# Kernel tuning notes

Hardware: AMD Instinct MI355X
Metric: run time of the kernel (lower is better)

Reference implementation:

```python
import jax, jax.numpy as jnp
import numpy as np
import math

B, S, E, H = 2, 2048, 1024, 16
D = E // H          # d_k = 64 = n_qubits_per_head
F = 1024            # ffn_dim; MUST equal E for the original mixing to broadcast
LN_EPS = 1e-5


def _layernorm(x, g, b):
    m = jnp.mean(x, axis=-1, keepdims=True)
    v = jnp.var(x, axis=-1, keepdims=True)
    return (x - m) / jnp.sqrt(v + LN_EPS) * g + b


def _circuit_expvals(x):
    # Closed form of the variational circuit: RY(x_i) on wire i, RZ(theta_i),
    # CNOT chain (i -> i+1), measure PauliZ on each wire.
    # RZ is diagonal (no effect on Z probs); CNOT chain makes bit_i the XOR of
    # bits 0..i, so <Z_i> = prod_{j<=i} cos(x_j).
    return jnp.cumprod(jnp.cos(x), axis=-1)


def setup_inputs() -> dict:
    key = jax.random.key(0)
    ks = jax.random.split(key, 18)
    sc = 0.02
    inp = {
        "x": jax.random.normal(ks[0], (B, S, E), jnp.float32),
        "mask": jnp.ones((B, S), jnp.int32),
        "wq": jax.random.normal(ks[1], (E, E), jnp.float32) * sc,
        "wk": jax.random.normal(ks[2], (E, E), jnp.float32) * sc,
        "wv": jax.random.normal(ks[3], (E, E), jnp.float32) * sc,
        "wo": jax.random.normal(ks[4], (E, E), jnp.float32) * sc,
        "attn_param": jax.random.normal(ks[5], (D,), jnp.float32),   # RZ angles (no effect on expvals)
        "attn_qw": jnp.float32(0.5),
        "w1": jax.random.normal(ks[6], (E, F), jnp.float32) * sc,
        "b1": jnp.zeros((F,), jnp.float32),
        "w2": jax.random.normal(ks[7], (F, E), jnp.float32) * sc,
        "b2": jnp.zeros((E,), jnp.float32),
        "ffn_param": jax.random.normal(ks[8], (E,), jnp.float32),    # RZ angles (no effect on expvals)
        "ffn_qw": jnp.float32(0.5),
        "ln1_g": jnp.ones((E,), jnp.float32),
        "ln1_b": jnp.zeros((E,), jnp.float32),
        "ln2_g": jnp.ones((E,), jnp.float32),
        "ln2_b": jnp.zeros((E,), jnp.float32),
    }
    return inp


def reference(x, mask, wq, wk, wv, wo, attn_param, attn_qw,
              w1, b1, w2, b2, ffn_param, ffn_qw,
              ln1_g, ln1_b, ln2_g, ln2_b):
    b, s, _ = x.shape
    # ---- quantum attention sublayer (dropout inactive / eval mode) ----
    q = (x @ wq).reshape(b, s, H, D).transpose(0, 2, 1, 3)  # [b,h,s,d]
    k = (x @ wk).reshape(b, s, H, D).transpose(0, 2, 1, 3)
    v = (x @ wv).reshape(b, s, H, D).transpose(0, 2, 1, 3)
    scores = jnp.einsum("bhqd,bhkd->bhqk", q, k) / math.sqrt(D)
    scores = jnp.where(mask[:, None, None, :] == 0, -jnp.inf, scores)
    attn = jax.nn.softmax(scores, axis=-1)
    classical = jnp.einsum("bhqk,bhkd->bhqd", attn, v)
    quantum = _circuit_expvals(q)                             # [b,h,s,d]
    wgt = jax.nn.sigmoid(attn_qw)
    out = wgt * quantum + (1.0 - wgt) * classical
    attn_out = out.transpose(0, 2, 1, 3).reshape(b, s, E) @ wo
    x1 = _layernorm(x + attn_out, ln1_g, ln1_b)
    # ---- quantum feed-forward sublayer ----
    classical2 = jax.nn.relu(x1 @ w1 + b1)                    # [b,s,F]
    quantum2 = _circuit_expvals(x1)                           # [b,s,E] (E==F)
    wgt2 = jax.nn.sigmoid(ffn_qw)
    h = wgt2 * quantum2 + (1.0 - wgt2) * classical2
    ffn_out = h @ w2 + b2
    return _layernorm(x1 + ffn_out, ln2_g, ln2_b)
```

## Files before the change

kernel.cpp:

```cpp
#include <hip/hip_runtime.h>
#include <hip/hip_bf16.h>
#include <cmath>
#include <cstdint>


typedef __bf16 bf16_t;
typedef __bf16 bf16x8 __attribute__((ext_vector_type(8)));
typedef float f32x4 __attribute__((ext_vector_type(4)));
typedef unsigned short u16x4 __attribute__((ext_vector_type(4)));

#define DEV_INLINE __device__ __forceinline__
#define MB 1048576

DEV_INLINE void gload16(const void* g, void* lds) {
  __builtin_amdgcn_global_load_lds(
      (const __attribute__((address_space(1))) unsigned int*)g,
      (__attribute__((address_space(3))) unsigned int*)lds, 16, 0, 0);
}

DEV_INLINE unsigned short bf16_bits(float f) {
  bf16_t b = (bf16_t)f;
  return __builtin_bit_cast(unsigned short, b);
}

__global__ __launch_bounds__(256) void prep_kernel(
    const float* __restrict__ x, const float* __restrict__ wq,
    const float* __restrict__ wk, const float* __restrict__ wv,
    const float* __restrict__ wo, const float* __restrict__ w1,
    const float* __restrict__ w2, bf16_t* __restrict__ xc,
    bf16_t* __restrict__ wqkvT, bf16_t* __restrict__ wT3) {
  __shared__ bf16_t t[32][33];
  const int bid = blockIdx.x;
  if (bid < 2048) {
    const size_t i0 = ((size_t)bid * 256 + threadIdx.x) * 8;
    bf16x8 v;
#pragma unroll
    for (int j = 0; j < 8; ++j) v[j] = (bf16_t)x[i0 + j];
    *(bf16x8*)(xc + i0) = v;
    return;
  }
  const int grp = (bid - 2048) / 3072;
  const int tcb = (bid - 2048) - grp * 3072;
  const int mi = tcb >> 10;
  const float* src;
  bf16_t* dst;
  if (grp == 0) {
    src = (mi == 0) ? wq : (mi == 1) ? wk : wv;
    dst = wqkvT;
  } else {
    src = (mi == 0) ? wo : (mi == 1) ? w1 : w2;
    dst = wT3;
  }
  const int rem = tcb & 1023;
  const int bx = (rem & 31) * 32, by = (rem >> 5) * 32;
  const int tx = threadIdx.x & 31, ty = threadIdx.x >> 5;
#pragma unroll
  for (int i = 0; i < 4; ++i)
    t[ty + i * 8][tx] = (bf16_t)src[(size_t)(by + ty + i * 8) * 1024 + bx + tx];
  __syncthreads();
#pragma unroll
  for (int i = 0; i < 4; ++i)
    dst[(size_t)(mi * 1024 + bx + ty + i * 8) * 1024 + by + tx] = t[tx][ty + i * 8];
}

__global__ __launch_bounds__(256) void qkvvt_kernel(
    const bf16_t* __restrict__ xc, const bf16_t* __restrict__ wqkvT,
    bf16_t* __restrict__ qb, bf16_t* __restrict__ kb,
    bf16_t* __restrict__ vTb) {
  constexpr int K = 1024, BK = 64;
  __shared__ __align__(16) bf16_t As[128 * BK];
  __shared__ __align__(16) bf16_t Bs[128 * BK];

  const int tid = threadIdx.x;
  const int w = tid >> 6, lane = tid & 63;
  const int quad = lane >> 4, tc = lane & 15;
  const int bid = blockIdx.x;
  const int isqk = (bid < 512);
  int m0, n0;
  const bf16_t *Ab, *Bb;
  if (isqk) {
    n0 = (bid & 15) * 128;
    m0 = (bid >> 4) * 128;
    Ab = xc + (size_t)m0 * K;
    Bb = wqkvT + (size_t)n0 * K;
  } else {
    const int t = bid - 512;
    n0 = (t & 31) * 128;
    m0 = (t >> 5) * 128;
    Ab = wqkvT + (size_t)(2 * 1024 * 1024) + (size_t)m0 * K;
    Bb = xc + (size_t)n0 * K;
  }
  const int wm = (w >> 1) * 64, wn = (w & 1) * 64;
  const int srow = lane >> 3, scol = (lane & 7) * 8;

  f32x4 acc[4][4] = {};

  for (int k0 = 0; k0 < K; k0 += BK) {
    __syncthreads();
#pragma unroll
    for (int it = 0; it < 4; ++it) {
      const int rbase = w * 32 + it * 8;
      gload16(Ab + (size_t)(rbase + srow) * K + k0 + scol, &As[rbase * BK]);
      gload16(Bb + (size_t)(rbase + srow) * K + k0 + scol, &Bs[rbase * BK]);
    }
    __syncthreads();
#pragma unroll
    for (int ks = 0; ks < 2; ++ks) {
      bf16x8 af[4], bfv[4];
#pragma unroll
      for (int i = 0; i < 4; ++i)
        af[i] = *(const bf16x8*)&As[(wm + i * 16 + tc) * BK + ks * 32 + quad * 8];
#pragma unroll
      for (int j = 0; j < 4; ++j)
        bfv[j] = *(const bf16x8*)&Bs[(wn + j * 16 + tc) * BK + ks * 32 + quad * 8];
#pragma unroll
      for (int i = 0; i < 4; ++i)
#pragma unroll
        for (int j = 0; j < 4; ++j)
          acc[i][j] = __builtin_amdgcn_mfma_f32_16x16x32_bf16(af[i], bfv[j],
                                                              acc[i][j], 0, 0, 0);
    }
  }

#pragma unroll
  for (int i = 0; i < 4; ++i) {
#pragma unroll
    for (int j = 0; j < 4; ++j) {
      const int row0 = m0 + wm + i * 16 + quad * 4;
      const int col = n0 + wn + j * 16 + tc;
      if (isqk) {
        const int part = col >> 10, e = col & 1023, hh = e >> 6, d = e & 63;
        bf16_t* dst = part ? kb : qb;
#pragma unroll
        for (int r = 0; r < 4; ++r) {
          const int row = row0 + r;
          const int b = row >> 11, s = row & 2047;
          dst[((size_t)(b * 16 + hh) * 2048 + s) * 64 + d] = (bf16_t)acc[i][j][r];
        }
      } else {
        const int b = col >> 11, s = col & 2047;
#pragma unroll
        for (int r = 0; r < 4; ++r) {
          vTb[((size_t)(b * 1024 + row0 + r)) * 2048 + s] = (bf16_t)acc[i][j][r];
        }
      }
    }
  }
}

enum { EPI_WO = 2, EPI_W1 = 3, EPI_W2 = 4 };

template <int EPI>
__global__ __launch_bounds__(256) void gemm_bt_kernel(
    const bf16_t* __restrict__ A, const bf16_t* __restrict__ Bt,
    void* __restrict__ o0, const float* __restrict__ auxf,
    const bf16_t* __restrict__ auxb, const float* __restrict__ bias,
    const float* __restrict__ scal) {
  constexpr int K = 1024, BK = 64;
  __shared__ __align__(16) bf16_t As[64 * BK];
  __shared__ __align__(16) bf16_t Bs[64 * BK];

  const int tid = threadIdx.x;
  const int w = tid >> 6, lane = tid & 63;
  const int quad = lane >> 4, tc = lane & 15;
  const int m0 = blockIdx.y * 64, n0 = blockIdx.x * 64;
  const int wm = (w >> 1) * 32, wn = (w & 1) * 32;
  const int srow = lane >> 3, scol = (lane & 7) * 8;

  f32x4 acc[2][2] = {};

  const bf16_t* Ab = A + (size_t)m0 * K;
  const bf16_t* Bb = Bt + (size_t)n0 * K;

  for (int k0 = 0; k0 < K; k0 += BK) {
    __syncthreads();
#pragma unroll
    for (int it = 0; it < 2; ++it) {
      const int rbase = w * 16 + it * 8;
      gload16(Ab + (size_t)(rbase + srow) * K + k0 + scol, &As[rbase * BK]);
      gload16(Bb + (size_t)(rbase + srow) * K + k0 + scol, &Bs[rbase * BK]);
    }
    __syncthreads();
#pragma unroll
    for (int ks = 0; ks < 2; ++ks) {
      bf16x8 af[2], bfv[2];
#pragma unroll
      for (int i = 0; i < 2; ++i)
        af[i] = *(const bf16x8*)&As[(wm + i * 16 + tc) * BK + ks * 32 + quad * 8];
#pragma unroll
      for (int j = 0; j < 2; ++j)
        bfv[j] = *(const bf16x8*)&Bs[(wn + j * 16 + tc) * BK + ks * 32 + quad * 8];
#pragma unroll
      for (int i = 0; i < 2; ++i)
#pragma unroll
        for (int j = 0; j < 2; ++j)
          acc[i][j] = __builtin_amdgcn_mfma_f32_16x16x32_bf16(af[i], bfv[j],
                                                              acc[i][j], 0, 0, 0);
    }
  }

  float wsig = 0.f;
  if (EPI == EPI_W1) wsig = 1.f / (1.f + __expf(-scal[0]));

#pragma unroll
  for (int i = 0; i < 2; ++i) {
#pragma unroll
    for (int j = 0; j < 2; ++j) {
      const int row0 = m0 + wm + i * 16 + quad * 4;
      const int col = n0 + wn + j * 16 + tc;
      if (EPI == EPI_WO) {
#pragma unroll
        for (int r = 0; r < 4; ++r) {
          const int row = row0 + r;
          ((float*)o0)[(size_t)row * 1024 + col] =
              acc[i][j][r] + auxf[(size_t)row * 1024 + col];
        }
      } else if (EPI == EPI_W1) {
#pragma unroll
        for (int r = 0; r < 4; ++r) {
          const int row = row0 + r;
          float c = fmaxf(acc[i][j][r] + bias[col], 0.f);
          const float qv = (float)auxb[(size_t)row * 1024 + col];
          ((bf16_t*)o0)[(size_t)row * 1024 + col] =
              (bf16_t)(wsig * qv + (1.f - wsig) * c);
        }
      } else {
#pragma unroll
        for (int r = 0; r < 4; ++r) {
          const int row = row0 + r;
          ((float*)o0)[(size_t)row * 1024 + col] =
              acc[i][j][r] + bias[col] + (float)auxb[(size_t)row * 1024 + col];
        }
      }
    }
  }
}

__global__ __launch_bounds__(256) void attn_kernel(
    const bf16_t* __restrict__ q, const bf16_t* __restrict__ k,
    const bf16_t* __restrict__ vT, const float* __restrict__ aqw,
    bf16_t* __restrict__ out) {
  constexpr int S = 2048, LDK = 72;
  __shared__ __align__(16) bf16_t Ks[64 * LDK];
  __shared__ __align__(16) bf16_t Vs[64 * LDK];
  __shared__ __align__(16) bf16_t Ps[4][32 * LDK];
  __shared__ bf16_t Ql[128 * LDK];
  __shared__ float segp[128][4];

  const int tid = threadIdx.x, w = tid >> 6, lane = tid & 63;
  const int quad = lane >> 4, tc = lane & 15;
  const int bh = blockIdx.y, q0 = blockIdx.x * 128;
  const bf16_t* qg = q + ((size_t)bh * S + q0) * 64;
  const bf16_t* kg = k + (size_t)bh * S * 64;
  const bf16_t* vg = vT + (size_t)bh * 64 * S;

  const int strow = tid >> 2, stcol = (tid & 3) * 16;

  bf16x8 pk0 = *(const bf16x8*)(kg + (size_t)strow * 64 + stcol);
  bf16x8 pk1 = *(const bf16x8*)(kg + (size_t)strow * 64 + stcol + 8);
  bf16x8 pv0 = *(const bf16x8*)(vg + (size_t)strow * S + stcol);
  bf16x8 pv1 = *(const bf16x8*)(vg + (size_t)strow * S + stcol + 8);

  {
    float c[2][16];
    const int ss = tid & 3;
#pragma unroll
    for (int pass = 0; pass < 2; ++pass) {
      const int rr = pass * 64 + (tid >> 2);
      const bf16_t* qr = qg + rr * 64 + ss * 16;
      float p = 1.f;
#pragma unroll
      for (int j2 = 0; j2 < 16; ++j2) {
        c[pass][j2] = __cosf((float)qr[j2]);
        p *= c[pass][j2];
      }
      segp[rr][ss] = p;
    }
    __syncthreads();
#pragma unroll
    for (int pass = 0; pass < 2; ++pass) {
      const int rr = pass * 64 + (tid >> 2);
      float pre = 1.f;
      for (int u = 0; u < ss; ++u) pre *= segp[rr][u];
#pragma unroll
      for (int j2 = 0; j2 < 16; ++j2) {
        pre *= c[pass][j2];
        Ql[rr * LDK + ss * 16 + j2] = (bf16_t)pre;
      }
    }
  }

  bf16x8 aq[2][2];
#pragma unroll
  for (int qs = 0; qs < 2; ++qs) {
    const int qrow = w * 32 + qs * 16 + tc;
#pragma unroll
    for (int ks = 0; ks < 2; ++ks) {
      bf16x8 t = *(const bf16x8*)(qg + qrow * 64 + ks * 32 + quad * 8);
#pragma unroll
      for (int e = 0; e < 8; ++e) t[e] = (bf16_t)((float)t[e] * 0.18033688f);
      aq[qs][ks] = t;
    }
  }

  float lacc[2] = {0.f, 0.f};
  f32x4 o[2][4] = {};
  bf16_t* Pw = Ps[w];

  for (int kt = 0; kt < S; kt += 64) {
    __syncthreads();
    *(bf16x8*)&Ks[strow * LDK + stcol] = pk0;
    *(bf16x8*)&Ks[strow * LDK + stcol + 8] = pk1;
    *(bf16x8*)&Vs[strow * LDK + stcol] = pv0;
    *(bf16x8*)&Vs[strow * LDK + stcol + 8] = pv1;
    if (kt + 64 < S) {
      const int nk = kt + 64;
      pk0 = *(const bf16x8*)(kg + (size_t)(nk + strow) * 64 + stcol);
      pk1 = *(const bf16x8*)(kg + (size_t)(nk + strow) * 64 + stcol + 8);
      pv0 = *(const bf16x8*)(vg + (size_t)strow * S + nk + stcol);
      pv1 = *(const bf16x8*)(vg + (size_t)strow * S + nk + stcol + 8);
    }
    __syncthreads();

    f32x4 sf[2][4] = {};
#pragma unroll
    for (int ks = 0; ks < 2; ++ks) {
#pragma unroll
      for (int nt = 0; nt < 4; ++nt) {
        bf16x8 ak = *(const bf16x8*)&Ks[(nt * 16 + tc) * LDK + ks * 32 + quad * 8];
        sf[0][nt] = __builtin_amdgcn_mfma_f32_16x16x32_bf16(ak, aq[0][ks], sf[0][nt], 0, 0, 0);
        sf[1][nt] = __builtin_amdgcn_mfma_f32_16x16x32_bf16(ak, aq[1][ks], sf[1][nt], 0, 0, 0);
      }
    }

#pragma unroll
    for (int qs = 0; qs < 2; ++qs) {
#pragma unroll
      for (int nt = 0; nt < 4; ++nt) {
        u16x4 pk;
        float ps = 0.f;
#pragma unroll
        for (int r = 0; r < 4; ++r) {
          const float p = __builtin_amdgcn_exp2f(sf[qs][nt][r]);
          ps += p;
          pk[r] = bf16_bits(p);
        }
        lacc[qs] += ps;
        *(u16x4*)&Pw[(qs * 16 + tc) * LDK + nt * 16 + quad * 4] = pk;
      }
    }
    asm volatile("s_waitcnt lgkmcnt(0)" ::: "memory");

#pragma unroll
    for (int ks = 0; ks < 2; ++ks) {
      bf16x8 ap0 = *(const bf16x8*)&Pw[tc * LDK + ks * 32 + quad * 8];
      bf16x8 ap1 = *(const bf16x8*)&Pw[(16 + tc) * LDK + ks * 32 + quad * 8];
#pragma unroll
      for (int j = 0; j < 4; ++j) {
        bf16x8 bv = *(const bf16x8*)&Vs[(j * 16 + tc) * LDK + ks * 32 + quad * 8];
        o[0][j] = __builtin_amdgcn_mfma_f32_16x16x32_bf16(ap0, bv, o[0][j], 0, 0, 0);
        o[1][j] = __builtin_amdgcn_mfma_f32_16x16x32_bf16(ap1, bv, o[1][j], 0, 0, 0);
      }
    }
  }

#pragma unroll
  for (int qs = 0; qs < 2; ++qs) {
    lacc[qs] += __shfl_xor(lacc[qs], 16, 64);
    lacc[qs] += __shfl_xor(lacc[qs], 32, 64);
  }

  const float wsig = 1.f / (1.f + __expf(-aqw[0]));
  const int b = bh >> 4, h = bh & 15;
#pragma unroll
  for (int qs = 0; qs < 2; ++qs) {
#pragma unroll
    for (int r = 0; r < 4; ++r) {
      const int lr = quad * 4 + r;
      const float linv = 1.f / __shfl(lacc[qs], lr, 64);
      const int lrow = w * 32 + qs * 16 + lr;
      const int sg = q0 + lrow;
#pragma unroll
      for (int j = 0; j < 4; ++j) {
        const int d = j * 16 + tc;
        const float cl = o[qs][j][r] * linv;
        const float qv = (float)Ql[lrow * LDK + d];
        out[((size_t)(b * 2048 + sg)) * 1024 + h * 64 + d] =
            (bf16_t)(wsig * qv + (1.f - wsig) * cl);
      }
    }
  }
}

__global__ __launch_bounds__(256) void ln1scan_kernel(
    const float* __restrict__ res, const float* __restrict__ g,
    const float* __restrict__ bta, bf16_t* __restrict__ x1,
    bf16_t* __restrict__ q2) {
  const int row = blockIdx.x;
  const int tid = threadIdx.x, w = tid >> 6, lane = tid & 63;
  f32x4 v = *(const f32x4*)&res[(size_t)row * 1024 + tid * 4];
  float s = v[0] + v[1] + v[2] + v[3];
  float sq = v[0] * v[0] + v[1] * v[1] + v[2] * v[2] + v[3] * v[3];
#pragma unroll
  for (int off = 32; off >= 1; off >>= 1) {
    s += __shfl_xor(s, off, 64);
    sq += __shfl_xor(sq, off, 64);
  }
  __shared__ float rs[4], rq[4], wtot[4];
  if (lane == 0) {
    rs[w] = s;
    rq[w] = sq;
  }
  __syncthreads();
  s = rs[0] + rs[1] + rs[2] + rs[3];
  sq = rq[0] + rq[1] + rq[2] + rq[3];
  const float mean = s * (1.f / 1024.f);
  const float var = fmaxf(sq * (1.f / 1024.f) - mean * mean, 0.f);
  const float rstd = rsqrtf(var + 1e-5f);

  const f32x4 gv = *(const f32x4*)&g[tid * 4];
  const f32x4 bv = *(const f32x4*)&bta[tid * 4];
  float c[4], p = 1.f;
  u16x4 xb;
#pragma unroll
  for (int i = 0; i < 4; ++i) {
    const float y = (v[i] - mean) * rstd * gv[i] + bv[i];
    const bf16_t yb = (bf16_t)y;
    xb[i] = __builtin_bit_cast(unsigned short, yb);
    c[i] = __cosf((float)yb);
    p *= c[i];
  }
  *(u16x4*)&x1[(size_t)row * 1024 + tid * 4] = xb;

  float ip = p;
#pragma unroll
  for (int off = 1; off < 64; off <<= 1) {
    const float t = __shfl_up(ip, off, 64);
    if (lane >= off) ip *= t;
  }
  if (lane == 63) wtot[w] = ip;
  __syncthreads();
  float carry = 1.f;
  for (int u = 0; u < w; ++u) carry *= wtot[u];
  float run = __shfl_up(ip, 1, 64);
  if (lane == 0) run = 1.f;
  run *= carry;
  u16x4 qv;
#pragma unroll
  for (int i = 0; i < 4; ++i) {
    run *= c[i];
    qv[i] = bf16_bits(run);
  }
  *(u16x4*)&q2[(size_t)row * 1024 + tid * 4] = qv;
}

__global__ __launch_bounds__(256) void ln2_kernel(
    const float* __restrict__ res, const float* __restrict__ g,
    const float* __restrict__ bta, float* __restrict__ out) {
  const int row = blockIdx.x;
  const int tid = threadIdx.x, w = tid >> 6, lane = tid & 63;
  f32x4 v = *(const f32x4*)&res[(size_t)row * 1024 + tid * 4];
  float s = v[0] + v[1] + v[2] + v[3];
  float sq = v[0] * v[0] + v[1] * v[1] + v[2] * v[2] + v[3] * v[3];
#pragma unroll
  for (int off = 32; off >= 1; off >>= 1) {
    s += __shfl_xor(s, off, 64);
    sq += __shfl_xor(sq, off, 64);
  }
  __shared__ float rs[4], rq[4];
  if (lane == 0) {
    rs[w] = s;
    rq[w] = sq;
  }
  __syncthreads();
  s = rs[0] + rs[1] + rs[2] + rs[3];
  sq = rq[0] + rq[1] + rq[2] + rq[3];
  const float mean = s * (1.f / 1024.f);
  const float var = fmaxf(sq * (1.f / 1024.f) - mean * mean, 0.f);
  const float rstd = rsqrtf(var + 1e-5f);
  const f32x4 gv = *(const f32x4*)&g[tid * 4];
  const f32x4 bv = *(const f32x4*)&bta[tid * 4];
  f32x4 y;
#pragma unroll
  for (int i = 0; i < 4; ++i) y[i] = (v[i] - mean) * rstd * gv[i] + bv[i];
  *(f32x4*)&out[(size_t)row * 1024 + tid * 4] = y;
}

extern "C" void kernel_launch(void* const* d_in, const int* in_sizes, int n_in,
                              void* d_out, int out_size, void* d_ws,
                              size_t ws_size, hipStream_t stream) {
  (void)in_sizes;
  (void)n_in;
  (void)out_size;
  (void)ws_size;
  const float* x = (const float*)d_in[0];
  const float* wq = (const float*)d_in[2];
  const float* wk = (const float*)d_in[3];
  const float* wv = (const float*)d_in[4];
  const float* wo = (const float*)d_in[5];
  const float* attn_qw = (const float*)d_in[7];
  const float* w1 = (const float*)d_in[8];
  const float* b1 = (const float*)d_in[9];
  const float* w2 = (const float*)d_in[10];
  const float* b2 = (const float*)d_in[11];
  const float* ffn_qw = (const float*)d_in[13];
  const float* ln1_g = (const float*)d_in[14];
  const float* ln1_b = (const float*)d_in[15];
  const float* ln2_g = (const float*)d_in[16];
  const float* ln2_b = (const float*)d_in[17];

  char* ws = (char*)d_ws;
  char* wsout = (char*)d_out;
  bf16_t* wT3 = (bf16_t*)(ws + 0);
  bf16_t* wqkvT = (bf16_t*)(ws + 6 * MB);
  bf16_t* xc = (bf16_t*)(ws + 12 * MB);
  bf16_t* qb = (bf16_t*)(ws + 20 * MB);
  bf16_t* aout = (bf16_t*)(ws + 6 * MB);
  float* res = (float*)(ws + 14 * MB);
  bf16_t* x1 = (bf16_t*)(ws + 6 * MB);
  float* res2 = (float*)(ws + 14 * MB);
  bf16_t* kb = (bf16_t*)(wsout + 0);
  bf16_t* vTb = (bf16_t*)(wsout + 8 * MB);
  bf16_t* q2 = (bf16_t*)(wsout + 0);
  bf16_t* hbuf = (bf16_t*)(wsout + 8 * MB);

  const dim3 tb(256);

  prep_kernel<<<8192, tb, 0, stream>>>(x, wq, wk, wv, wo, w1, w2, xc, wqkvT, wT3);

  qkvvt_kernel<<<768, tb, 0, stream>>>(xc, wqkvT, qb, kb, vTb);

  attn_kernel<<<dim3(16, 32), tb, 0, stream>>>(qb, kb, vTb, attn_qw, aout);

  gemm_bt_kernel<EPI_WO><<<dim3(16, 64), tb, 0, stream>>>(
      aout, wT3, res, x, nullptr, nullptr, nullptr);

  ln1scan_kernel<<<4096, tb, 0, stream>>>(res, ln1_g, ln1_b, x1, q2);

  gemm_bt_kernel<EPI_W1><<<dim3(16, 64), tb, 0, stream>>>(
      x1, wT3 + 1024 * 1024, hbuf, nullptr, q2, b1, ffn_qw);

  gemm_bt_kernel<EPI_W2><<<dim3(16, 64), tb, 0, stream>>>(
      hbuf, wT3 + 2 * 1024 * 1024, res2, nullptr, x1, b2, nullptr);

  ln2_kernel<<<4096, tb, 0, stream>>>(res2, ln2_g, ln2_b, (float*)d_out);
}
```

Before: 286.7 us.

## Load attention K/V fragments directly to registers and store residuals in bf16

The attention kernel drops the K and V shared-memory tiles and their per-tile barriers. Each lane now loads its MFMA fragments straight from global memory into registers, double-buffering K across two 64-key tiles. Separately, the residual outputs of the Wo and W2 GEMMs are written as bf16 instead of fp32, the Wo residual reads the bf16 copy of x, and both layernorm kernels read bf16. This cuts global traffic and synchronisation, at the cost of more register pressure, uncoalesced fragment loads, and lower residual precision before layernorm.

Result: slower. 356.2 us (+24.3%).

```diff
diff --git a/kernel.cpp b/kernel.cpp
--- a/kernel.cpp
+++ b/kernel.cpp
@@ -21,6 +21,10 @@
 DEV_INLINE unsigned short bf16_bits(float f) {
   bf16_t b = (bf16_t)f;
   return __builtin_bit_cast(unsigned short, b);
+}
+
+DEV_INLINE float bf16_val(unsigned short u) {
+  return (float)__builtin_bit_cast(bf16_t, u);
 }
 
 __global__ __launch_bounds__(256) void prep_kernel(
@@ -153,9 +157,8 @@
 template <int EPI>
 __global__ __launch_bounds__(256) void gemm_bt_kernel(
     const bf16_t* __restrict__ A, const bf16_t* __restrict__ Bt,
-    void* __restrict__ o0, const float* __restrict__ auxf,
-    const bf16_t* __restrict__ auxb, const float* __restrict__ bias,
-    const float* __restrict__ scal) {
+    bf16_t* __restrict__ o0, const bf16_t* __restrict__ auxb,
+    const float* __restrict__ bias, const float* __restrict__ scal) {
   constexpr int K = 1024, BK = 64;
   __shared__ __align__(16) bf16_t As[64 * BK];
   __shared__ __align__(16) bf16_t Bs[64 * BK];
@@ -208,28 +211,18 @@
     for (int j = 0; j < 2; ++j) {
       const int row0 = m0 + wm + i * 16 + quad * 4;
       const int col = n0 + wn + j * 16 + tc;
-      if (EPI == EPI_WO) {
-#pragma unroll
-        for (int r = 0; r < 4; ++r) {
-          const int row = row0 + r;
-          ((float*)o0)[(size_t)row * 1024 + col] =
-              acc[i][j][r] + auxf[(size_t)row * 1024 + col];
-        }
-      } else if (EPI == EPI_W1) {
-#pragma unroll
-        for (int r = 0; r < 4; ++r) {
-          const int row = row0 + r;
+#pragma unroll
+      for (int r = 0; r < 4; ++r) {
+        const int row = row0 + r;
+        const size_t idx = (size_t)row * 1024 + col;
+        if (EPI == EPI_WO) {
+          o0[idx] = (bf16_t)(acc[i][j][r] + (float)auxb[idx]);
+        } else if (EPI == EPI_W1) {
           float c = fmaxf(acc[i][j][r] + bias[col], 0.f);
-          const float qv = (float)auxb[(size_t)row * 1024 + col];
-          ((bf16_t*)o0)[(size_t)row * 1024 + col] =
-              (bf16_t)(wsig * qv + (1.f - wsig) * c);
-        }
-      } else {
-#pragma unroll
-        for (int r = 0; r < 4; ++r) {
-          const int row = row0 + r;
-          ((float*)o0)[(size_t)row * 1024 + col] =
-              acc[i][j][r] + bias[col] + (float)auxb[(size_t)row * 1024 + col];
+          const float qv = (float)auxb[idx];
+          o0[idx] = (bf16_t)(wsig * qv + (1.f - wsig) * c);
+        } else {
+          o0[idx] = (bf16_t)(acc[i][j][r] + bias[col] + (float)auxb[idx]);
         }
       }
     }
@@ -241,8 +234,6 @@
     const bf16_t* __restrict__ vT, const float* __restrict__ aqw,
     bf16_t* __restrict__ out) {
   constexpr int S = 2048, LDK = 72;
-  __shared__ __align__(16) bf16_t Ks[64 * LDK];
-  __shared__ __align__(16) bf16_t Vs[64 * LDK];
   __shared__ __align__(16) bf16_t Ps[4][32 * LDK];
   __shared__ bf16_t Ql[128 * LDK];
   __shared__ float segp[128][4];
@@ -254,12 +245,15 @@
   const bf16_t* kg = k + (size_t)bh * S * 64;
   const bf16_t* vg = vT + (size_t)bh * 64 * S;
 
-  const int strow = tid >> 2, stcol = (tid & 3) * 16;
-
-  bf16x8 pk0 = *(const bf16x8*)(kg + (size_t)strow * 64 + stcol);
-  bf16x8 pk1 = *(const bf16x8*)(kg + (size_t)strow * 64 + stcol + 8);
-  bf16x8 pv0 = *(const bf16x8*)(vg + (size_t)strow * S + stcol);
-  bf16x8 pv1 = *(const bf16x8*)(vg + (size_t)strow * S + stcol + 8);
+  const bf16_t* kbase = kg + tc * 64 + quad * 8;
+  const bf16_t* vbase = vg + (size_t)tc * S + quad * 8;
+
+  bf16x8 kfA[8], kfB[8];
+#pragma unroll
+  for (int i = 0; i < 8; ++i) {
+    const int ks = i >> 2, nt = i & 3;
+    kfA[i] = *(const bf16x8*)(kbase + (size_t)(nt * 16) * 64 + ks * 32);
+  }
 
   {
     float c[2][16];
@@ -289,6 +283,7 @@
       }
     }
   }
+  __syncthreads();
 
   bf16x8 aq[2][2];
 #pragma unroll
@@ -307,32 +302,27 @@
   f32x4 o[2][4] = {};
   bf16_t* Pw = Ps[w];
 
-  for (int kt = 0; kt < S; kt += 64) {
-    __syncthreads();
-    *(bf16x8*)&Ks[strow * LDK + stcol] = pk0;
-    *(bf16x8*)&Ks[strow * LDK + stcol + 8] = pk1;
-    *(bf16x8*)&Vs[strow * LDK + stcol] = pv0;
-    *(bf16x8*)&Vs[strow * LDK + stcol + 8] = pv1;
-    if (kt + 64 < S) {
-      const int nk = kt + 64;
-      pk0 = *(const bf16x8*)(kg + (size_t)(nk + strow) * 64 + stcol);
-      pk1 = *(const bf16x8*)(kg + (size_t)(nk + strow) * 64 + stcol + 8);
-      pv0 = *(const bf16x8*)(vg + (size_t)strow * S + nk + stcol);
-      pv1 = *(const bf16x8*)(vg + (size_t)strow * S + nk + stcol + 8);
-    }
-    __syncthreads();
-
+  auto tile = [&](int kt, bf16x8* kf, bf16x8* kfn, int nkt) {
+    bf16x8 vf[8];
+#pragma unroll
+    for (int i = 0; i < 8; ++i) {
+      const int ks = i >> 2, j = i & 3;
+      vf[i] = *(const bf16x8*)(vbase + (size_t)(j * 16) * S + kt + ks * 32);
+    }
+#pragma unroll
+    for (int i = 0; i < 8; ++i) {
+      const int ks = i >> 2, nt = i & 3;
+      kfn[i] = *(const bf16x8*)(kbase + (size_t)(nkt + nt * 16) * 64 + ks * 32);
+    }
     f32x4 sf[2][4] = {};
 #pragma unroll
     for (int ks = 0; ks < 2; ++ks) {
 #pragma unroll
       for (int nt = 0; nt < 4; ++nt) {
-        bf16x8 ak = *(const bf16x8*)&Ks[(nt * 16 + tc) * LDK + ks * 32 + quad * 8];
-        sf[0][nt] = __builtin_amdgcn_mfma_f32_16x16x32_bf16(ak, aq[0][ks], sf[0][nt], 0, 0, 0);
-        sf[1][nt] = __builtin_amdgcn_mfma_f32_16x16x32_bf16(ak, aq[1][ks], sf[1][nt], 0, 0, 0);
-      }
-    }
-
+        sf[0][nt] = __builtin_amdgcn_mfma_f32_16x16x32_bf16(kf[ks * 4 + nt], aq[0][ks], sf[0][nt], 0, 0, 0);
+        sf[1][nt] = __builtin_amdgcn_mfma_f32_16x16x32_bf16(kf[ks * 4 + nt], aq[1][ks], sf[1][nt], 0, 0, 0);
+      }
+    }
 #pragma unroll
     for (int qs = 0; qs < 2; ++qs) {
 #pragma unroll
@@ -350,18 +340,21 @@
       }
     }
     asm volatile("s_waitcnt lgkmcnt(0)" ::: "memory");
-
 #pragma unroll
     for (int ks = 0; ks < 2; ++ks) {
       bf16x8 ap0 = *(const bf16x8*)&Pw[tc * LDK + ks * 32 + quad * 8];
       bf16x8 ap1 = *(const bf16x8*)&Pw[(16 + tc) * LDK + ks * 32 + quad * 8];
 #pragma unroll
       for (int j = 0; j < 4; ++j) {
-        bf16x8 bv = *(const bf16x8*)&Vs[(j * 16 + tc) * LDK + ks * 32 + quad * 8];
-        o[0][j] = __builtin_amdgcn_mfma_f32_16x16x32_bf16(ap0, bv, o[0][j], 0, 0, 0);
-        o[1][j] = __builtin_amdgcn_mfma_f32_16x16x32_bf16(ap1, bv, o[1][j], 0, 0, 0);
-      }
-    }
+        o[0][j] = __builtin_amdgcn_mfma_f32_16x16x32_bf16(ap0, vf[ks * 4 + j], o[0][j], 0, 0, 0);
+        o[1][j] = __builtin_amdgcn_mfma_f32_16x16x32_bf16(ap1, vf[ks * 4 + j], o[1][j], 0, 0, 0);
+      }
+    }
+  };
+
+  for (int kt = 0; kt < S; kt += 128) {
+    tile(kt, kfA, kfB, kt + 64);
+    tile(kt + 64, kfB, kfA, (kt + 128) & (S - 1));
   }
 
 #pragma unroll
@@ -393,12 +386,15 @@
 }
 
 __global__ __launch_bounds__(256) void ln1scan_kernel(
-    const float* __restrict__ res, const float* __restrict__ g,
+    const bf16_t* __restrict__ res, const float* __restrict__ g,
     const float* __restrict__ bta, bf16_t* __restrict__ x1,
     bf16_t* __restrict__ q2) {
   const int row = blockIdx.x;
   const int tid = threadIdx.x, w = tid >> 6, lane = tid & 63;
-  f32x4 v = *(const f32x4*)&res[(size_t)row * 1024 + tid * 4];
+  const u16x4 raw = *(const u16x4*)&res[(size_t)row * 1024 + tid * 4];
+  f32x4 v;
+#pragma unroll
+  for (int i = 0; i < 4; ++i) v[i] = bf16_val(raw[i]);
   float s = v[0] + v[1] + v[2] + v[3];
   float sq = v[0] * v[0] + v[1] * v[1] + v[2] * v[2] + v[3] * v[3];
 #pragma unroll
@@ -455,11 +451,14 @@
 }
 
 __global__ __launch_bounds__(256) void ln2_kernel(
-    const float* __restrict__ res, const float* __restrict__ g,
+    const bf16_t* __restrict__ res, const float* __restrict__ g,
     const float* __restrict__ bta, float* __restrict__ out) {
   const int row = blockIdx.x;
   const int tid = threadIdx.x, w = tid >> 6, lane = tid & 63;
-  f32x4 v = *(const f32x4*)&res[(size_t)row * 1024 + tid * 4];
+  const u16x4 raw = *(const u16x4*)&res[(size_t)row * 1024 + tid * 4];
+  f32x4 v;
+#pragma unroll
+  for (int i = 0; i < 4; ++i) v[i] = bf16_val(raw[i]);
   float s = v[0] + v[1] + v[2] + v[3];
   float sq = v[0] * v[0] + v[1] * v[1] + v[2] * v[2] + v[3] * v[3];
 #pragma unroll
@@ -513,12 +512,12 @@
   char* wsout = (char*)d_out;
   bf16_t* wT3 = (bf16_t*)(ws + 0);
   bf16_t* wqkvT = (bf16_t*)(ws + 6 * MB);
-  bf16_t* xc = (bf16_t*)(ws + 12 * MB);
-  bf16_t* qb = (bf16_t*)(ws + 20 * MB);
   bf16_t* aout = (bf16_t*)(ws + 6 * MB);
-  float* res = (float*)(ws + 14 * MB);
+  bf16_t* qb = (bf16_t*)(ws + 14 * MB);
+  bf16_t* xc = (bf16_t*)(ws + 22 * MB);
+  bf16_t* res = (bf16_t*)(ws + 14 * MB);
   bf16_t* x1 = (bf16_t*)(ws + 6 * MB);
-  float* res2 = (float*)(ws + 14 * MB);
+  bf16_t* res2 = (bf16_t*)(ws + 14 * MB);
   bf16_t* kb = (bf16_t*)(wsout + 0);
   bf16_t* vTb = (bf16_t*)(wsout + 8 * MB);
   bf16_t* q2 = (bf16_t*)(wsout + 0);
@@ -533,15 +532,15 @@
   attn_kernel<<<dim3(16, 32), tb, 0, stream>>>(qb, kb, vTb, attn_qw, aout);
 
   gemm_bt_kernel<EPI_WO><<<dim3(16, 64), tb, 0, stream>>>(
-      aout, wT3, res, x, nullptr, nullptr, nullptr);
+      aout, wT3, res, xc, nullptr, nullptr);
 
   ln1scan_kernel<<<4096, tb, 0, stream>>>(res, ln1_g, ln1_b, x1, q2);
 
   gemm_bt_kernel<EPI_W1><<<dim3(16, 64), tb, 0, stream>>>(
-      x1, wT3 + 1024 * 1024, hbuf, nullptr, q2, b1, ffn_qw);
+      x1, wT3 + 1024 * 1024, hbuf, q2, b1, ffn_qw);
 
   gemm_bt_kernel<EPI_W2><<<dim3(16, 64), tb, 0, stream>>>(
-      hbuf, wT3 + 2 * 1024 * 1024, res2, nullptr, x1, b2, nullptr);
+      hbuf, wT3 + 2 * 1024 * 1024, res2, x1, b2, nullptr);
 
   ln2_kernel<<<4096, tb, 0, stream>>>(res2, ln2_g, ln2_b, (float*)d_out);
 }
```
